# Performance work log

Measured on AMD Instinct MI355X. Metric: run time of the kernel, lower is better.

Reference implementation:

```python
import jax, jax.numpy as jnp
import numpy as np

K = 20          # knn neighbors (args.k)
BN_EPS = 1e-5   # torch BatchNorm default
LN_EPS = 1e-6


def _bn(x, g, b, axes):
    # training-mode batchnorm over `axes`, channel dim = 1
    m = x.mean(axes, keepdims=True)
    v = x.var(axes, keepdims=True)
    shp = [1] * x.ndim
    shp[1] = x.shape[1]
    return g.reshape(shp) * (x - m) * jax.lax.rsqrt(v + BN_EPS) + b.reshape(shp)


def _lrelu(x):
    return jnp.where(x >= 0, x, 0.2 * x)


def _graph_feature(x, k):
    # x: [B,C,N] -> [B,2C,N,k]  (knn gather + (neighbor-center, center) concat)
    B, C, N = x.shape
    inner = -2.0 * jnp.einsum('bcn,bcm->bnm', x, x)
    xx = jnp.sum(x * x, axis=1)                       # [B,N]
    pd = -xx[:, :, None] - inner - xx[:, None, :]     # negative sq. distance
    idx = jax.lax.top_k(pd, k)[1]                     # [B,N,k]
    xt = jnp.transpose(x, (0, 2, 1))                  # [B,N,C]
    feat = xt[jnp.arange(B)[:, None, None], idx]      # [B,N,k,C] gather
    ctr = xt[:, :, None, :]
    out = jnp.concatenate([feat - ctr, jnp.broadcast_to(ctr, feat.shape)], axis=-1)
    return jnp.transpose(out, (0, 3, 1, 2))


def _conv2d_block(x, w, g, b):
    # 1x1 conv2d (no bias) + BN2d + LeakyReLU(0.2)
    y = jnp.einsum('bcnk,oc->bonk', x, w)
    return _lrelu(_bn(y, g, b, (0, 2, 3)))


def _conv1d_block(x, w, g, b):
    y = jnp.einsum('bcl,oc->bol', x, w)
    return _lrelu(_bn(y, g, b, (0, 2)))


def _squash(t):
    sn = jnp.sum(t * t, axis=-1, keepdims=True)
    return sn * t / ((1.0 + sn) * jnp.sqrt(sn))


def _forward(data, l, dw1, dg1, db1, dw2, dg2, db2, dw3, dg3, db3,
             lin_w, ln_w, ln_b, caps_W,
             cw1, cg1, cb1, cw2, cg2, cb2, cw3, cw4, cg4, cb4, cw5, cg5, cb5):
    B, _, N = data.shape
    # ---- DGCNN encoder ----
    x = _conv2d_block(_graph_feature(data, K), dw1, dg1, db1)
    x1 = x.max(axis=-1)                               # [B,64,N]
    x = _conv2d_block(_graph_feature(x1, K), dw2, dg2, db2)
    x2 = x.max(axis=-1)                               # [B,64,N]
    x = _conv2d_block(_graph_feature(x2, K), dw3, dg3, db3)
    x3 = x.max(axis=-1)                               # [B,128,N]
    feat = jnp.transpose(jnp.concatenate([x1, x2, x3], axis=1), (0, 2, 1))  # [B,N,256]
    h = jnp.einsum('bnc,oc->bno', feat, lin_w)        # [B,N,40]
    mu = h.mean(axis=(1, 2), keepdims=True)
    var = h.var(axis=(1, 2), keepdims=True)
    encoder = jax.nn.relu(ln_w * (h - mu) * jax.lax.rsqrt(var + LN_EPS) + ln_b)  # [B,1024,40]
    # ---- Latent capsule layer (3-iter dynamic routing) ----
    u_hat = jnp.einsum('lpvd,bpd->blpv', caps_W, encoder)  # [B,40,1024,64]
    u_det = jax.lax.stop_gradient(u_hat)
    b_ij = jnp.zeros((B, caps_W.shape[0], caps_W.shape[1]), encoder.dtype)
    v = None
    for it in range(3):
        c = jax.nn.softmax(b_ij, axis=1)
        if it == 2:
            v = _squash(jnp.einsum('blp,blpv->blv', c, u_hat))
        else:
            v = _squash(jnp.einsum('blp,blpv->blv', c, u_det))
            b_ij = b_ij + jnp.einsum('blv,blpv->blp', v, u_det)
    latent = v                                        # [B,40,64]
    # ---- segmentation head ----
    emb = jnp.einsum('bpd,bdv->bpv', encoder, latent) # [B,1024,64]
    emb = emb.max(axis=-1, keepdims=True)             # [B,1024,1]
    lab = _conv1d_block(l.reshape(B, -1, 1), cw1, cg1, cb1)  # [B,64,1]
    emb = jnp.concatenate([emb, lab], axis=1)         # [B,1088,1]
    emb = jnp.tile(emb, (1, 1, N))                    # [B,1088,N]
    emb = jnp.concatenate([emb, jnp.transpose(encoder, (0, 2, 1))], axis=1)  # [B,1128,N]
    r = _conv1d_block(emb, cw2, cg2, cb2)
    r = _conv1d_block(r, cw3, cg2, cb2)               # conv3 shares bn2 params
    r = _conv1d_block(r, cw4, cg4, cb4)
    r = _conv1d_block(r, cw5, cg5, cb5)
    return r                                          # [B,50,N]


def setup_inputs() -> dict:
    key = jax.random.key(0)
    ks = jax.random.split(key, 16)
    B, N = 32, 1024
    f = jnp.float32
    rn = lambda k, s: 0.05 * jax.random.normal(k, s, dtype=f)
    return dict(
        data=jax.random.normal(ks[0], (B, 3, N), dtype=f),
        l=jax.random.uniform(ks[1], (B, 16), dtype=f),
        dw1=rn(ks[2], (64, 6)), dg1=jnp.ones(64, f), db1=jnp.zeros(64, f),
        dw2=rn(ks[3], (64, 128)), dg2=jnp.ones(64, f), db2=jnp.zeros(64, f),
        dw3=rn(ks[4], (128, 128)), dg3=jnp.ones(128, f), db3=jnp.zeros(128, f),
        lin_w=rn(ks[5], (40, 256)),
        ln_w=jnp.ones((N, 40), f), ln_b=jnp.zeros((N, 40), f),
        caps_W=0.01 * jax.random.normal(ks[6], (40, 1024, 64, 40), dtype=f),
        cw1=rn(ks[7], (64, 16)), cg1=jnp.ones(64, f), cb1=jnp.zeros(64, f),
        cw2=rn(ks[8], (256, 1128)), cg2=jnp.ones(256, f), cb2=jnp.zeros(256, f),
        cw3=rn(ks[9], (256, 256)),
        cw4=rn(ks[10], (128, 256)), cg4=jnp.ones(128, f), cb4=jnp.zeros(128, f),
        cw5=rn(ks[11], (50, 128)), cg5=jnp.ones(50, f), cb5=jnp.zeros(50, f),
    )


def reference(data, l, dw1, dg1, db1, dw2, dg2, db2, dw3, dg3, db3,
              lin_w, ln_w, ln_b, caps_W,
              cw1, cg1, cb1, cw2, cg2, cb2, cw3, cw4, cg4, cb4, cw5, cg5, cb5):
    return _forward(data, l, dw1, dg1, db1, dw2, dg2, db2, dw3, dg3, db3,
                    lin_w, ln_w, ln_b, caps_W,
                    cw1, cg1, cb1, cw2, cg2, cb2, cw3, cw4, cg4, cb4, cw5, cg5, cb5)
```

## Files before the change

### kernel.cpp

```cpp
#include <hip/hip_runtime.h>
#include <math.h>

constexpr int NB = 32, NN = 1024, KNN = 20;
constexpr int RTOT = NB * NN;

constexpr size_t SZ_BIG = (size_t)NB * NN * 40 * 64;
constexpr size_t O_BIG  = 0;
constexpr size_t O_XT0  = O_BIG + SZ_BIG;
constexpr size_t O_XT1  = O_XT0 + (size_t)RTOT * 4;
constexpr size_t O_XT2  = O_XT1 + (size_t)RTOT * 64;
constexpr size_t O_XT3  = O_XT2 + (size_t)RTOT * 64;
constexpr size_t O_XX   = O_XT3 + (size_t)RTOT * 128;
constexpr size_t O_IDX  = O_XX + RTOT;
constexpr size_t O_WC1  = O_IDX + (size_t)RTOT * KNN;
constexpr size_t O_WC2  = O_WC1 + 512;
constexpr size_t O_WC3  = O_WC2 + 8192;
constexpr size_t O_LWT  = O_WC3 + 16384;
constexpr size_t O_C2T  = O_LWT + 16384;
constexpr size_t O_C3T  = O_C2T + 10240;
constexpr size_t O_C4T  = O_C3T + 65536;
constexpr size_t O_C5T  = O_C4T + 32768;
constexpr size_t O_H    = O_C5T + 8192;
constexpr size_t O_LNST = O_H + (size_t)RTOT * 64;
constexpr size_t O_BSUM = O_LNST + 64;
constexpr size_t O_BSQ  = O_BSUM + 256;
constexpr size_t O_SCL  = O_BSQ + 256;
constexpr size_t O_SHF  = O_SCL + 256;
constexpr size_t O_SACC = O_SHF + 256;
constexpr size_t O_VB   = O_SACC + 81920;
constexpr size_t O_BIJ  = O_VB + 81920;
constexpr size_t O_EMB  = O_BIJ + (size_t)NB * 40 * NN;
constexpr size_t O_LAB  = O_EMB + RTOT;
constexpr size_t O_BASE = O_LAB + 2048;
constexpr size_t O_PS   = O_BIJ;
constexpr size_t O_PQ   = O_BIJ + 262144;
constexpr size_t O_PB   = O_XT1;
constexpr size_t O_PBU  = O_XT1;

__device__ __forceinline__ float lrelu(float z) { return fmaxf(z, 0.2f * z); }

__device__ __forceinline__ float key2f(unsigned u)
{
    unsigned b = (u & 0x80000000u) ? (u ^ 0x80000000u) : ~u;
    return __uint_as_float(b);
}

__global__ void k_wt(const float* __restrict__ src, float* __restrict__ dst,
                     int K, int On, int SS, int coff, int DS, int ooff, int Oreal)
{
    int i = blockIdx.x * 256 + threadIdx.x;
    if (i >= K * On) return;
    int c = i / On, o = i - c * On;
    dst[(size_t)c * DS + ooff + o] = (o < Oreal) ? src[(size_t)o * SS + coff + c] : 0.f;
}

__global__ void k_data_t(const float* __restrict__ d, float* __restrict__ xt)
{
    int i = blockIdx.x * 256 + threadIdx.x;
    if (i >= RTOT) return;
    int b = i >> 10, n = i & 1023;
#pragma unroll
    for (int c = 0; c < 3; ++c) xt[(size_t)i * 4 + c] = d[((size_t)b * 3 + c) * NN + n];
    xt[(size_t)i * 4 + 3] = 0.f;
}

template<int C, int CS>
__global__ void k_rownorm(const float* __restrict__ X, float* __restrict__ xx)
{
    int i = blockIdx.x * 256 + threadIdx.x;
    if (i >= RTOT) return;
    const float* p = X + (size_t)i * CS;
    float s = 0.f;
#pragma unroll
    for (int c = 0; c < C; ++c) s = fmaf(p[c], p[c], s);
    xx[i] = s;
}

template<int CS>
__global__ __launch_bounds__(256) void k_dist(const float* __restrict__ X,
    const float* __restrict__ xx, float* __restrict__ D)
{
    __shared__ float As[16][68];
    __shared__ float Bs[16][68];
    int b = blockIdx.z;
    int r0 = blockIdx.x * 64, m0 = blockIdx.y * 64;
    const float* Xb = X + (size_t)b * NN * CS;
    int t = threadIdx.x;
    int tx = t & 15, ty = t >> 4;
    float acc[4][4] = {};
    for (int k0 = 0; k0 < CS; k0 += 16) {
        __syncthreads();
        {
            int row = t >> 2, kb = (t & 3) * 4;
#pragma unroll
            for (int u = 0; u < 4; ++u) {
                int k = k0 + kb + u;
                As[kb + u][row] = (k < CS) ? Xb[(size_t)(r0 + row) * CS + k] : 0.f;
                Bs[kb + u][row] = (k < CS) ? Xb[(size_t)(m0 + row) * CS + k] : 0.f;
            }
        }
        __syncthreads();
#pragma unroll
        for (int k = 0; k < 16; ++k) {
            float4 a = *(const float4*)&As[k][ty * 4];
            float4 bb = *(const float4*)&Bs[k][tx * 4];
            float av[4] = {a.x, a.y, a.z, a.w};
            float bv[4] = {bb.x, bb.y, bb.z, bb.w};
#pragma unroll
            for (int i = 0; i < 4; ++i)
#pragma unroll
                for (int j = 0; j < 4; ++j)
                    acc[i][j] = fmaf(av[i], bv[j], acc[i][j]);
        }
    }
    const float* xxb = xx + b * NN + m0 + tx * 4;
    float x0 = xxb[0], x1 = xxb[1], x2 = xxb[2], x3 = xxb[3];
#pragma unroll
    for (int i = 0; i < 4; ++i) {
        float4 o4 = make_float4(2.f * acc[i][0] - x0, 2.f * acc[i][1] - x1,
                                2.f * acc[i][2] - x2, 2.f * acc[i][3] - x3);
        *(float4*)&D[((size_t)b * NN + r0 + ty * 4 + i) * NN + m0 + tx * 4] = o4;
    }
}

__global__ __launch_bounds__(256) void k_sel(const float* __restrict__ D,
                                             int* __restrict__ idxb)
{
    int gw = blockIdx.x * 4 + (threadIdx.x >> 6);
    int lane = threadIdx.x & 63;
    const float* drow = D + (size_t)gw * NN;
    float vr[16];
#pragma unroll
    for (int j = 0; j < 16; ++j) vr[j] = drow[j * 64 + lane];

    unsigned lo = 0x007FFFFFu;
    unsigned hi = 0xFF800000u;
#pragma unroll 1
    while (hi - lo > 1u) {
        unsigned mid = lo + ((hi - lo) >> 1);
        float tm = key2f(mid);
        int c = 0;
#pragma unroll
        for (int j = 0; j < 16; ++j) c += __popcll(__ballot(vr[j] > tm));
        if (c < KNN) hi = mid; else lo = mid;
    }
    float t = key2f(hi);

    int* outp = idxb + (size_t)gw * KNN;
    unsigned long long mylow = (1ull << lane) - 1ull;
    int base = 0;
#pragma unroll
    for (int j = 0; j < 16; ++j) {
        unsigned long long bmask = __ballot(vr[j] > t);
        if (vr[j] > t) outp[base + __popcll(bmask & mylow)] = j * 64 + lane;
        base += __popcll(bmask);
    }
#pragma unroll 1
    for (int j = 0; j < 16 && base < KNN; ++j) {
        unsigned long long bmask = __ballot(vr[j] == t);
        int pre = __popcll(bmask & mylow);
        if (vr[j] == t && base + pre < KNN) outp[base + pre] = j * 64 + lane;
        base += __popcll(bmask);
    }
}

template<bool ACT, bool BIAS>
__global__ __launch_bounds__(256) void k_gemm(const float* __restrict__ X,
    const float* __restrict__ W, float* __restrict__ Y, int K, int OC, int XS,
    const float* __restrict__ scale, const float* __restrict__ shift,
    const float* __restrict__ bias)
{
    __shared__ float Xs[16][68];
    __shared__ float Ws[16][64];
    int r0 = blockIdx.x * 64, o0 = blockIdx.y * 64;
    int t = threadIdx.x;
    int tx = t & 15, ty = t >> 4;
    float acc[4][4] = {};
    for (int k0 = 0; k0 < K; k0 += 16) {
        __syncthreads();
        {
            int row = t >> 2, kb = (t & 3) * 4;
#pragma unroll
            for (int u = 0; u < 4; ++u) {
                int k = k0 + kb + u;
                float v = 0.f;
                if (k < K) {
                    v = X[(size_t)(r0 + row) * XS + k];
                    if (ACT) { float z = fmaf(v, scale[k], shift[k]); v = fmaxf(z, 0.2f * z); }
                }
                Xs[kb + u][row] = v;
            }
            int kw = t >> 4, ow = (t & 15) * 4;
            float4 wv = make_float4(0.f, 0.f, 0.f, 0.f);
            if (k0 + kw < K) wv = *(const float4*)&W[(size_t)(k0 + kw) * OC + o0 + ow];
            *(float4*)&Ws[kw][ow] = wv;
        }
        __syncthreads();
#pragma unroll
        for (int k = 0; k < 16; ++k) {
            float4 a = *(const float4*)&Xs[k][ty * 4];
            float4 bb = *(const float4*)&Ws[k][tx * 4];
            float av[4] = {a.x, a.y, a.z, a.w};
            float bvv[4] = {bb.x, bb.y, bb.z, bb.w};
#pragma unroll
            for (int i = 0; i < 4; ++i)
#pragma unroll
                for (int j = 0; j < 4; ++j)
                    acc[i][j] = fmaf(av[i], bvv[j], acc[i][j]);
        }
    }
#pragma unroll
    for (int i = 0; i < 4; ++i) {
        int r = r0 + ty * 4 + i;
        float4 o4;
        float* po = (float*)&o4;
#pragma unroll
        for (int j = 0; j < 4; ++j) {
            float v = acc[i][j];
            if (BIAS) v += bias[(size_t)(r >> 10) * OC + o0 + tx * 4 + j];
            po[j] = v;
        }
        *(float4*)&Y[(size_t)r * OC + o0 + tx * 4] = o4;
    }
}

template<int O>
__global__ __launch_bounds__(256) void k_gather(const float* __restrict__ Z,
    const int* __restrict__ idxb, float* __restrict__ xo,
    float* __restrict__ part_s, float* __restrict__ part_q)
{
    constexpr int OL = O / 64;
    __shared__ float rs[4][O], rq[4][O];
    int b = blockIdx.y, nt = blockIdx.x;
    int t = threadIdx.x, lane = t & 63, w = t >> 6;
    float ps[OL] = {}, pq[OL] = {};
    for (int i = 0; i < 4; ++i) {
        int n = nt * 16 + w * 4 + i;
        size_t r = (size_t)b * NN + n;
        float zd[OL], ym[OL];
#pragma unroll
        for (int j = 0; j < OL; ++j) {
            int o = lane + j * 64;
            zd[j] = Z[r * (2 * O) + O + o] - Z[r * (2 * O) + o];
            ym[j] = -3.4e38f;
        }
        int midx[KNN];
        {
            const int4* ip = (const int4*)&idxb[r * KNN];
#pragma unroll
            for (int q = 0; q < 5; ++q) {
                int4 t4 = ip[q];
                midx[4 * q + 0] = t4.x; midx[4 * q + 1] = t4.y;
                midx[4 * q + 2] = t4.z; midx[4 * q + 3] = t4.w;
            }
        }
#pragma unroll
        for (int k = 0; k < KNN; ++k) {
            size_t rm = (size_t)b * NN + midx[k];
#pragma unroll
            for (int j = 0; j < OL; ++j) {
                float y = Z[rm * (2 * O) + lane + j * 64] + zd[j];
                ym[j] = fmaxf(ym[j], y);
                ps[j] += y; pq[j] = fmaf(y, y, pq[j]);
            }
        }
#pragma unroll
        for (int j = 0; j < OL; ++j) xo[r * O + lane + j * 64] = ym[j];
    }
#pragma unroll
    for (int j = 0; j < OL; ++j) { rs[w][lane + j * 64] = ps[j]; rq[w][lane + j * 64] = pq[j]; }
    __syncthreads();
    if (w == 0) {
        int blk = blockIdx.y * 64 + blockIdx.x;
#pragma unroll
        for (int j = 0; j < OL; ++j) {
            int o = lane + j * 64;
            part_s[(size_t)o * 2048 + blk] = rs[0][o] + rs[1][o] + rs[2][o] + rs[3][o];
            part_q[(size_t)o * 2048 + blk] = rq[0][o] + rq[1][o] + rq[2][o] + rq[3][o];
        }
    }
}

__global__ void k_bnfin2(const float* __restrict__ part_s, const float* __restrict__ part_q,
                         const float* __restrict__ g, const float* __restrict__ bb,
                         float* __restrict__ scale, float* __restrict__ shift,
                         int OC, float invM, float eps)
{
    int o = blockIdx.x * blockDim.x + threadIdx.x;
    if (o >= OC) return;
    const float* ps = part_s + (size_t)o * 2048;
    const float* pq = part_q + (size_t)o * 2048;
    float s0 = 0.f, s1 = 0.f, s2 = 0.f, s3 = 0.f;
    float q0 = 0.f, q1 = 0.f, q2 = 0.f, q3 = 0.f;
    for (int i = 0; i < 2048; i += 4) {
        s0 += ps[i]; s1 += ps[i + 1]; s2 += ps[i + 2]; s3 += ps[i + 3];
        q0 += pq[i]; q1 += pq[i + 1]; q2 += pq[i + 2]; q3 += pq[i + 3];
    }
    float s = (s0 + s1) + (s2 + s3);
    float q = (q0 + q1) + (q2 + q3);
    float mu = s * invM;
    float var = q * invM - mu * mu;
    float sc = g[o] * rsqrtf(var + eps);
    scale[o] = sc; shift[o] = bb[o] - mu * sc;
}

__global__ void k_bnfin(const float* __restrict__ sums, const float* __restrict__ sumsq,
                        const float* __restrict__ g, const float* __restrict__ bb,
                        float* __restrict__ scale, float* __restrict__ shift,
                        int OC, float invM, float eps)
{
    int o = blockIdx.x * blockDim.x + threadIdx.x;
    if (o >= OC) return;
    float mu = sums[o] * invM;
    float var = sumsq[o] * invM - mu * mu;
    float sc = g[o] * rsqrtf(var + eps);
    scale[o] = sc; shift[o] = bb[o] - mu * sc;
}

__global__ void k_bnapply(float* __restrict__ x, const float* __restrict__ scale,
                          const float* __restrict__ shift, int total, int O)
{
    int i = blockIdx.x * 256 + threadIdx.x;
    if (i >= total) return;
    int o = i & (O - 1);
    x[i] = lrelu(fmaf(x[i], scale[o], shift[o]));
}

__global__ void k_concat(const float* __restrict__ x1, const float* __restrict__ x2,
                         const float* __restrict__ x3, float* __restrict__ f)
{
    int i = blockIdx.x * 256 + threadIdx.x;
    if (i >= RTOT * 256) return;
    int r = i >> 8, c = i & 255;
    float v;
    if (c < 64) v = x1[(size_t)r * 64 + c];
    else if (c < 128) v = x2[(size_t)r * 64 + c - 64];
    else v = x3[(size_t)r * 128 + c - 128];
    f[(size_t)i] = v;
}

__global__ __launch_bounds__(256) void k_lnstats(const float* __restrict__ h, float* __restrict__ st)
{
    __shared__ float rsm[256], rqm[256];
    int b = blockIdx.x, t = threadIdx.x;
    float s = 0.f, q = 0.f;
    for (int i = t; i < 40960; i += 256) {
        int n = i / 40, o = i - n * 40;
        float v = h[((size_t)b * NN + n) * 64 + o];
        s += v; q = fmaf(v, v, q);
    }
    rsm[t] = s; rqm[t] = q; __syncthreads();
    for (int off = 128; off; off >>= 1) {
        if (t < off) { rsm[t] += rsm[t + off]; rqm[t] += rqm[t + off]; }
        __syncthreads();
    }
    if (t == 0) {
        float mu = rsm[0] / 40960.f;
        float var = rqm[0] / 40960.f - mu * mu;
        st[2 * b] = mu; st[2 * b + 1] = rsqrtf(var + 1e-6f);
    }
}

__global__ void k_lnapply(float* __restrict__ h, const float* __restrict__ lnw,
                          const float* __restrict__ lnb, const float* __restrict__ st)
{
    int i = blockIdx.x * 256 + threadIdx.x;
    if (i >= NB * NN * 40) return;
    int b = i / 40960, rem = i - b * 40960, n = rem / 40, o = rem - n * 40;
    float mu = st[2 * b], rstd = st[2 * b + 1];
    size_t a = ((size_t)b * NN + n) * 64 + o;
    float v = fmaf((h[a] - mu) * rstd, lnw[n * 40 + o], lnb[n * 40 + o]);
    h[a] = fmaxf(v, 0.f);
}

__global__ __launch_bounds__(128) void k_uhat(const float* __restrict__ enc,
    const float* __restrict__ caps, float* __restrict__ U, float* __restrict__ pbu)
{
    __shared__ float clt[2][40 * 68];
    __shared__ float red[2048];
    int pc = blockIdx.x, l = blockIdx.y;
    int t = threadIdx.x, lane = t & 63, wv = t >> 6;
    int vg = lane & 7, bg = lane >> 3;
    int v0 = vg * 8, b0 = bg * 4;
    float* cw = clt[wv];
    float spart[4][8] = {};
#pragma unroll 1
    for (int pi = 0; pi < 8; ++pi) {
        int p = pc * 16 + wv * 8 + pi;
        const float4* cp4 = (const float4*)(caps + ((size_t)l * NN + p) * 2560);
#pragma unroll
        for (int k = 0; k < 10; ++k) {
            int i4 = lane + k * 64;
            float4 cv = cp4[i4];
            int e0 = i4 * 4;
            int v = e0 / 40;
            int d0 = e0 - v * 40;
            cw[(d0 + 0) * 68 + v] = cv.x;
            cw[(d0 + 1) * 68 + v] = cv.y;
            cw[(d0 + 2) * 68 + v] = cv.z;
            cw[(d0 + 3) * 68 + v] = cv.w;
        }
        float acc[4][8] = {};
#pragma unroll
        for (int d4 = 0; d4 < 10; ++d4) {
            float4 e4[4];
#pragma unroll
            for (int i = 0; i < 4; ++i)
                e4[i] = *(const float4*)&enc[((size_t)(b0 + i) * NN + p) * 64 + d4 * 4];
#pragma unroll
            for (int dd = 0; dd < 4; ++dd) {
                int d = d4 * 4 + dd;
                float4 c0 = *(const float4*)&cw[d * 68 + v0];
                float4 c1 = *(const float4*)&cw[d * 68 + v0 + 4];
                float cv[8] = {c0.x, c0.y, c0.z, c0.w, c1.x, c1.y, c1.z, c1.w};
#pragma unroll
                for (int i = 0; i < 4; ++i) {
                    float e = ((const float*)&e4[i])[dd];
#pragma unroll
                    for (int j = 0; j < 8; ++j)
                        acc[i][j] = fmaf(e, cv[j], acc[i][j]);
                }
            }
        }
#pragma unroll
        for (int i = 0; i < 4; ++i) {
            float* up = &U[((size_t)(b0 + i) * NN + p) * 2560 + l * 64 + v0];
            float4 o0 = make_float4(acc[i][0], acc[i][1], acc[i][2], acc[i][3]);
            float4 o1 = make_float4(acc[i][4], acc[i][5], acc[i][6], acc[i][7]);
            *(float4*)up = o0;
            *(float4*)(up + 4) = o1;
#pragma unroll
            for (int j = 0; j < 8; ++j) spart[i][j] += acc[i][j];
        }
    }
    if (wv == 1) {
#pragma unroll
        for (int i = 0; i < 4; ++i)
#pragma unroll
            for (int j = 0; j < 8; ++j)
                red[(b0 + i) * 64 + v0 + j] = spart[i][j];
    }
    __syncthreads();
    if (wv == 0) {
        float* pb = pbu + (size_t)pc * 81920;
#pragma unroll
        for (int i = 0; i < 4; ++i)
#pragma unroll
            for (int j = 0; j < 8; ++j) {
                int bv = (b0 + i) * 64 + v0 + j;
                pb[(size_t)(b0 + i) * 2560 + l * 64 + v0 + j] = spart[i][j] + red[bv];
            }
    }
}

template<int MODE>
__global__ __launch_bounds__(256, 4) void k_route(const float* __restrict__ U,
    const float* __restrict__ vprev, const float* __restrict__ bin,
    float* __restrict__ bout, float* __restrict__ pbuf)
{
    __shared__ float vl[2560];
    __shared__ float red[4][1280];
    int b = blockIdx.x, pc = blockIdx.y;
    int t = threadIdx.x, lane = t & 63, w = t >> 6;
    for (int i = t; i < 2560; i += 256) vl[i] = vprev[(size_t)b * 2560 + i];
    __syncthreads();
    float4 acc[10];
#pragma unroll
    for (int it = 0; it < 10; ++it) acc[it] = make_float4(0.f, 0.f, 0.f, 0.f);
    int lgrp = lane >> 4;
#pragma unroll 1
    for (int pi = 0; pi < 8; ++pi) {
        int p = pc * 32 + w * 8 + pi;
        const float4* up4 = (const float4*)(U + ((size_t)b * NN + p) * 2560);
        float4 u[10];
#pragma unroll
        for (int it = 0; it < 10; ++it) u[it] = up4[it * 64 + lane];
        float pd[10];
#pragma unroll
        for (int it = 0; it < 10; ++it) {
            float4 vv = *(const float4*)&vl[it * 256 + lane * 4];
            float s = u[it].x * vv.x;
            s = fmaf(u[it].y, vv.y, s);
            s = fmaf(u[it].z, vv.z, s);
            s = fmaf(u[it].w, vv.w, s);
            s += __shfl_xor(s, 1, 64);
            s += __shfl_xor(s, 2, 64);
            s += __shfl_xor(s, 4, 64);
            s += __shfl_xor(s, 8, 64);
            pd[it] = s;
        }
        if (MODE == 1) {
            if ((lane & 15) == 0) {
#pragma unroll
                for (int it = 0; it < 10; ++it)
                    bout[((size_t)b * 40 + it * 4 + lgrp) * NN + p] = pd[it];
            }
        } else {
#pragma unroll
            for (int it = 0; it < 10; ++it)
                pd[it] += bin[((size_t)b * 40 + it * 4 + lgrp) * NN + p];
        }
        float mx = -3.4e38f;
#pragma unroll
        for (int it = 0; it < 10; ++it) {
            float m = pd[it];
            m = fmaxf(m, __shfl_xor(m, 16, 64));
            m = fmaxf(m, __shfl_xor(m, 32, 64));
            mx = fmaxf(mx, m);
        }
        float eo[10]; float se = 0.f;
#pragma unroll
        for (int it = 0; it < 10; ++it) {
            float e = expf(pd[it] - mx);
            eo[it] = e;
            float sg = e;
            sg += __shfl_xor(sg, 16, 64);
            sg += __shfl_xor(sg, 32, 64);
            se += sg;
        }
        float inv = 1.f / se;
#pragma unroll
        for (int it = 0; it < 10; ++it) {
            float wgt = eo[it] * inv;
            acc[it].x = fmaf(wgt, u[it].x, acc[it].x);
            acc[it].y = fmaf(wgt, u[it].y, acc[it].y);
            acc[it].z = fmaf(wgt, u[it].z, acc[it].z);
            acc[it].w = fmaf(wgt, u[it].w, acc[it].w);
        }
    }
    float* pb = pbuf + ((size_t)pc * NB + b) * 2560;
#pragma unroll 1
    for (int h = 0; h < 2; ++h) {
        __syncthreads();
#pragma unroll
        for (int it = 0; it < 5; ++it)
            *(float4*)&red[w][it * 256 + lane * 4] = acc[h * 5 + it];
        __syncthreads();
        if (w == 0) {
#pragma unroll
            for (int it = 0; it < 5; ++it) {
                int idx = it * 256 + lane * 4;
                float4 a0 = *(const float4*)&red[0][idx];
                float4 a1 = *(const float4*)&red[1][idx];
                float4 a2 = *(const float4*)&red[2][idx];
                float4 a3 = *(const float4*)&red[3][idx];
                float4 o = make_float4((a0.x + a1.x) + (a2.x + a3.x),
                                       (a0.y + a1.y) + (a2.y + a3.y),
                                       (a0.z + a1.z) + (a2.z + a3.z),
                                       (a0.w + a1.w) + (a2.w + a3.w));
                *(float4*)&pb[h * 1280 + idx] = o;
            }
        }
    }
}

template<int NCH>
__global__ void k_sredN(const float* __restrict__ pbuf, float* __restrict__ sac)
{
    int i4 = blockIdx.x * 256 + threadIdx.x;
    if (i4 >= NB * 640) return;
    const float4* pb4 = (const float4*)pbuf;
    float4 s = make_float4(0.f, 0.f, 0.f, 0.f);
#pragma unroll 4
    for (int pc = 0; pc < NCH; ++pc) {
        float4 v = pb4[(size_t)pc * (NB * 640) + i4];
        s.x += v.x; s.y += v.y; s.z += v.z; s.w += v.w;
    }
    ((float4*)sac)[i4] = s;
}

__global__ void k_squash(const float* __restrict__ s_in, float* __restrict__ vout, float premul)
{
    int i = blockIdx.x * 256 + threadIdx.x;
    if (i >= NB * 40) return;
    const float* sp = s_in + (size_t)i * 64;
    float* vp = vout + (size_t)i * 64;
    float sn = 0.f;
    for (int v = 0; v < 64; ++v) { float tv = sp[v] * premul; sn = fmaf(tv, tv, sn); }
    float f = sn / ((1.f + sn) * sqrtf(sn));
    for (int v = 0; v < 64; ++v) vp[v] = sp[v] * premul * f;
}

__global__ __launch_bounds__(256) void k_emb(const float* __restrict__ enc,
    const float* __restrict__ lat, float* __restrict__ embm)
{
    __shared__ float latl[2560];
    int b = blockIdx.x, pt = blockIdx.y;
    int t = threadIdx.x, lane = t & 63, w = t >> 6;
    for (int i = t; i < 2560; i += 256) latl[i] = lat[(size_t)b * 2560 + i];
    __syncthreads();
    for (int i = 0; i < 32; ++i) {
        int p = pt * 128 + w * 32 + i;
        const float* ep = enc + ((size_t)b * NN + p) * 64;
        float acc = 0.f;
#pragma unroll
        for (int d = 0; d < 40; ++d) acc = fmaf(ep[d], latl[d * 64 + lane], acc);
        float mx = acc;
#pragma unroll
        for (int s = 32; s; s >>= 1) mx = fmaxf(mx, __shfl_xor(mx, s, 64));
        if (lane == 0) embm[(size_t)b * NN + p] = mx;
    }
}

__global__ __launch_bounds__(64) void k_lab(const float* __restrict__ lin,
    const float* __restrict__ w, const float* __restrict__ g, const float* __restrict__ bb,
    float* __restrict__ lab)
{
    int o = threadIdx.x;
    float ys[32]; float s = 0.f, q = 0.f;
#pragma unroll
    for (int b = 0; b < 32; ++b) {
        float y = 0.f;
#pragma unroll
        for (int c = 0; c < 16; ++c) y = fmaf(lin[b * 16 + c], w[o * 16 + c], y);
        ys[b] = y; s += y; q = fmaf(y, y, q);
    }
    float mu = s / 32.f, var = q / 32.f - mu * mu;
    float sc = g[o] * rsqrtf(var + 1e-5f);
    float sh = bb[o] - mu * sc;
#pragma unroll
    for (int b = 0; b < 32; ++b) lab[b * 64 + o] = lrelu(fmaf(ys[b], sc, sh));
}

__global__ __launch_bounds__(256) void k_base2(const float* __restrict__ em,
    const float* __restrict__ lab, const float* __restrict__ cw2, float* __restrict__ base)
{
    __shared__ float eml[1024];
    __shared__ float lbl[64];
    int b = blockIdx.x, t = threadIdx.x;
    for (int i = t; i < 1024; i += 256) eml[i] = em[(size_t)b * NN + i];
    if (t < 64) lbl[t] = lab[b * 64 + t];
    __syncthreads();
    const float* wr = cw2 + (size_t)t * 1128;
    float acc = 0.f;
    for (int c = 0; c < 1024; ++c) acc = fmaf(wr[c], eml[c], acc);
#pragma unroll
    for (int c = 0; c < 64; ++c) acc = fmaf(wr[1024 + c], lbl[c], acc);
    base[b * 256 + t] = acc;
}

__global__ __launch_bounds__(256) void k_colstats(const float* __restrict__ Y,
    float* __restrict__ sums, float* __restrict__ sumsq, int OC)
{
    __shared__ float rs[4][64], rq[4][64];
    int chunk = blockIdx.x, o0 = blockIdx.y * 64;
    int t = threadIdx.x, lane = t & 63, w = t >> 6;
    int o = o0 + lane;
    float s = 0.f, q = 0.f;
    for (int j = 0; j < 64; ++j) {
        int r = chunk * 256 + w * 64 + j;
        float v = Y[(size_t)r * OC + o];
        s += v; q = fmaf(v, v, q);
    }
    rs[w][lane] = s; rq[w][lane] = q;
    __syncthreads();
    if (w == 0) {
        atomicAdd(&sums[o], rs[0][lane] + rs[1][lane] + rs[2][lane] + rs[3][lane]);
        atomicAdd(&sumsq[o], rq[0][lane] + rq[1][lane] + rq[2][lane] + rq[3][lane]);
    }
}

__global__ void k_out(const float* __restrict__ Y, const float* __restrict__ scale,
                      const float* __restrict__ shift, float* __restrict__ out)
{
    int i = blockIdx.x * 256 + threadIdx.x;
    if (i >= NB * 50 * NN) return;
    int n = i & 1023, rest = i >> 10;
    int o = rest % 50, b = rest / 50;
    float y = Y[((size_t)b * NN + n) * 64 + o];
    out[i] = lrelu(fmaf(y, scale[o], shift[o]));
}

extern "C" void kernel_launch(void* const* d_in, const int* in_sizes, int n_in,
                              void* d_out, int out_size, void* d_ws, size_t ws_size,
                              hipStream_t stream)
{
    const float* data = (const float*)d_in[0];
    const float* lin  = (const float*)d_in[1];
    const float* dw1  = (const float*)d_in[2];
    const float* dg1  = (const float*)d_in[3];
    const float* db1  = (const float*)d_in[4];
    const float* dw2  = (const float*)d_in[5];
    const float* dg2  = (const float*)d_in[6];
    const float* db2  = (const float*)d_in[7];
    const float* dw3  = (const float*)d_in[8];
    const float* dg3  = (const float*)d_in[9];
    const float* db3  = (const float*)d_in[10];
    const float* lw   = (const float*)d_in[11];
    const float* lnw  = (const float*)d_in[12];
    const float* lnb  = (const float*)d_in[13];
    const float* caps = (const float*)d_in[14];
    const float* cw1  = (const float*)d_in[15];
    const float* cg1  = (const float*)d_in[16];
    const float* cb1  = (const float*)d_in[17];
    const float* cw2  = (const float*)d_in[18];
    const float* cg2  = (const float*)d_in[19];
    const float* cb2  = (const float*)d_in[20];
    const float* cw3  = (const float*)d_in[21];
    const float* cw4  = (const float*)d_in[22];
    const float* cg4  = (const float*)d_in[23];
    const float* cb4  = (const float*)d_in[24];
    const float* cw5  = (const float*)d_in[25];
    const float* cg5  = (const float*)d_in[26];
    const float* cb5  = (const float*)d_in[27];
    float* out = (float*)d_out;
    float* ws = (float*)d_ws;

    float* big  = ws + O_BIG;
    float* xt0  = ws + O_XT0;
    float* xt1  = ws + O_XT1;
    float* xt2  = ws + O_XT2;
    float* xt3  = ws + O_XT3;
    float* xxp  = ws + O_XX;
    int*   idxb = (int*)(ws + O_IDX);
    float* wc1  = ws + O_WC1;
    float* wc2  = ws + O_WC2;
    float* wc3  = ws + O_WC3;
    float* lwt  = ws + O_LWT;
    float* c2t  = ws + O_C2T;
    float* c3t  = ws + O_C3T;
    float* c4t  = ws + O_C4T;
    float* c5t  = ws + O_C5T;
    float* hbuf = ws + O_H;
    float* lnst = ws + O_LNST;
    float* bsum = ws + O_BSUM;
    float* bsq  = ws + O_BSQ;
    float* scl  = ws + O_SCL;
    float* shf  = ws + O_SHF;
    float* sac  = ws + O_SACC;
    float* vb   = ws + O_VB;
    float* bij  = ws + O_BIJ;
    float* embm = ws + O_EMB;
    float* labp = ws + O_LAB;
    float* basep= ws + O_BASE;
    float* psP  = ws + O_PS;
    float* pqP  = ws + O_PQ;
    float* pbuf = ws + O_PB;
    float* pbu  = ws + O_PBU;
    float* Dbuf = big;
    float* Z    = big;
    float* U    = big;
    float* yb1  = big;
    float* yb2  = big + 8388608;

    k_wt<<<1,   256, 0, stream>>>(dw1, wc1, 3, 64, 6, 0, 128, 0, 64);
    k_wt<<<1,   256, 0, stream>>>(dw1, wc1, 3, 64, 6, 3, 128, 64, 64);
    k_wt<<<16,  256, 0, stream>>>(dw2, wc2, 64, 64, 128, 0, 128, 0, 64);
    k_wt<<<16,  256, 0, stream>>>(dw2, wc2, 64, 64, 128, 64, 128, 64, 64);
    k_wt<<<32,  256, 0, stream>>>(dw3, wc3, 64, 128, 128, 0, 256, 0, 128);
    k_wt<<<32,  256, 0, stream>>>(dw3, wc3, 64, 128, 128, 64, 256, 128, 128);
    k_wt<<<64,  256, 0, stream>>>(lw,  lwt, 256, 64, 256, 0, 64, 0, 40);
    k_wt<<<40,  256, 0, stream>>>(cw2, c2t, 40, 256, 1128, 1088, 256, 0, 256);
    k_wt<<<256, 256, 0, stream>>>(cw3, c3t, 256, 256, 256, 0, 256, 0, 256);
    k_wt<<<128, 256, 0, stream>>>(cw4, c4t, 256, 128, 256, 0, 128, 0, 128);
    k_wt<<<32,  256, 0, stream>>>(cw5, c5t, 128, 64, 128, 0, 64, 0, 50);
    k_data_t<<<128, 256, 0, stream>>>(data, xt0);

    k_rownorm<3, 4><<<128, 256, 0, stream>>>(xt0, xxp);
    k_dist<4><<<dim3(16, 16, 32), 256, 0, stream>>>(xt0, xxp, Dbuf);
    k_sel<<<8192, 256, 0, stream>>>(Dbuf, idxb);
    k_gemm<false, false><<<dim3(512, 2), 256, 0, stream>>>(xt0, wc1, Z, 3, 128, 4, nullptr, nullptr, nullptr);
    k_gather<64><<<dim3(64, 32), 256, 0, stream>>>(Z, idxb, xt1, psP, pqP);
    k_bnfin2<<<1, 64, 0, stream>>>(psP, pqP, dg1, db1, scl, shf, 64, 1.f / 655360.f, 1e-5f);
    k_bnapply<<<8192, 256, 0, stream>>>(xt1, scl, shf, RTOT * 64, 64);

    k_rownorm<64, 64><<<128, 256, 0, stream>>>(xt1, xxp);
    k_dist<64><<<dim3(16, 16, 32), 256, 0, stream>>>(xt1, xxp, Dbuf);
    k_sel<<<8192, 256, 0, stream>>>(Dbuf, idxb);
    k_gemm<false, false><<<dim3(512, 2), 256, 0, stream>>>(xt1, wc2, Z, 64, 128, 64, nullptr, nullptr, nullptr);
    k_gather<64><<<dim3(64, 32), 256, 0, stream>>>(Z, idxb, xt2, psP, pqP);
    k_bnfin2<<<1, 64, 0, stream>>>(psP, pqP, dg2, db2, scl, shf, 64, 1.f / 655360.f, 1e-5f);
    k_bnapply<<<8192, 256, 0, stream>>>(xt2, scl, shf, RTOT * 64, 64);

    k_rownorm<64, 64><<<128, 256, 0, stream>>>(xt2, xxp);
    k_dist<64><<<dim3(16, 16, 32), 256, 0, stream>>>(xt2, xxp, Dbuf);
    k_sel<<<8192, 256, 0, stream>>>(Dbuf, idxb);
    k_gemm<false, false><<<dim3(512, 4), 256, 0, stream>>>(xt2, wc3, Z, 64, 256, 64, nullptr, nullptr, nullptr);
    k_gather<128><<<dim3(64, 32), 256, 0, stream>>>(Z, idxb, xt3, psP, pqP);
    k_bnfin2<<<1, 128, 0, stream>>>(psP, pqP, dg3, db3, scl, shf, 128, 1.f / 655360.f, 1e-5f);
    k_bnapply<<<16384, 256, 0, stream>>>(xt3, scl, shf, RTOT * 128, 128);

    k_concat<<<32768, 256, 0, stream>>>(xt1, xt2, xt3, big);
    k_gemm<false, false><<<dim3(512, 1), 256, 0, stream>>>(big, lwt, hbuf, 256, 64, 256, nullptr, nullptr, nullptr);
    k_lnstats<<<32, 256, 0, stream>>>(hbuf, lnst);
    k_lnapply<<<5120, 256, 0, stream>>>(hbuf, lnw, lnb, lnst);

    k_uhat<<<dim3(64, 40), 128, 0, stream>>>(hbuf, caps, U, pbu);
    k_sredN<64><<<80, 256, 0, stream>>>(pbu, sac);
    k_squash<<<5, 256, 0, stream>>>(sac, vb, 1.f / 40.f);
    k_route<1><<<dim3(32, 32), 256, 0, stream>>>(U, vb, nullptr, bij, pbuf);
    k_sredN<32><<<80, 256, 0, stream>>>(pbuf, sac);
    k_squash<<<5, 256, 0, stream>>>(sac, vb, 1.f);
    k_route<2><<<dim3(32, 32), 256, 0, stream>>>(U, vb, bij, nullptr, pbuf);
    k_sredN<32><<<80, 256, 0, stream>>>(pbuf, sac);
    k_squash<<<5, 256, 0, stream>>>(sac, vb, 1.f);

    k_emb<<<dim3(32, 8), 256, 0, stream>>>(hbuf, vb, embm);
    k_lab<<<1, 64, 0, stream>>>(lin, cw1, cg1, cb1, labp);
    k_base2<<<32, 256, 0, stream>>>(embm, labp, cw2, basep);

    k_gemm<false, true><<<dim3(512, 4), 256, 0, stream>>>(hbuf, c2t, yb1, 40, 256, 64, nullptr, nullptr, basep);
    hipMemsetAsync(bsum, 0, 512 * 4, stream);
    k_colstats<<<dim3(128, 4), 256, 0, stream>>>(yb1, bsum, bsq, 256);
    k_bnfin<<<1, 256, 0, stream>>>(bsum, bsq, cg2, cb2, scl, shf, 256, 1.f / 32768.f, 1e-5f);

    k_gemm<true, false><<<dim3(512, 4), 256, 0, stream>>>(yb1, c3t, yb2, 256, 256, 256, scl, shf, nullptr);
    hipMemsetAsync(bsum, 0, 512 * 4, stream);
    k_colstats<<<dim3(128, 4), 256, 0, stream>>>(yb2, bsum, bsq, 256);
    k_bnfin<<<1, 256, 0, stream>>>(bsum, bsq, cg2, cb2, scl, shf, 256, 1.f / 32768.f, 1e-5f);

    k_gemm<true, false><<<dim3(512, 2), 256, 0, stream>>>(yb2, c4t, yb1, 256, 128, 256, scl, shf, nullptr);
    hipMemsetAsync(bsum, 0, 512 * 4, stream);
    k_colstats<<<dim3(128, 2), 256, 0, stream>>>(yb1, bsum, bsq, 128);
    k_bnfin<<<1, 256, 0, stream>>>(bsum, bsq, cg4, cb4, scl, shf, 128, 1.f / 32768.f, 1e-5f);

    k_gemm<true, false><<<dim3(512, 1), 256, 0, stream>>>(yb1, c5t, yb2, 128, 64, 128, scl, shf, nullptr);
    hipMemsetAsync(bsum, 0, 512 * 4, stream);
    k_colstats<<<dim3(128, 1), 256, 0, stream>>>(yb2, bsum, bsq, 64);
    k_bnfin<<<1, 256, 0, stream>>>(bsum, bsq, cg5, cb5, scl, shf, 50, 1.f / 32768.f, 1e-5f);

    k_out<<<6400, 256, 0, stream>>>(yb2, scl, shf, out);
}
```

Before: 1.765 ms.

## Fuse kNN distance computation with top-k selection in shared memory

Replaces the separate tiled distance GEMM and the top-k selection kernel with one kernel. Each block computes distance rows for 8 points into shared memory and then runs the existing ballot-based threshold search on them. This removes writing and re-reading a full B×N×N distance matrix in global memory for each of the three graph layers. In exchange, the distance computation loses the 2D register tiling, so every block streams all candidate points from cache, which raises L2 traffic and lowers arithmetic reuse.

```diff
diff --git a/kernel.cpp b/kernel.cpp
--- a/kernel.cpp
+++ b/kernel.cpp
@@ -76,91 +76,74 @@
     xx[i] = s;
 }
 
-template<int CS>
-__global__ __launch_bounds__(256) void k_dist(const float* __restrict__ X,
-    const float* __restrict__ xx, float* __restrict__ D)
-{
-    __shared__ float As[16][68];
-    __shared__ float Bs[16][68];
-    int b = blockIdx.z;
-    int r0 = blockIdx.x * 64, m0 = blockIdx.y * 64;
+template<int CS, int CV>
+__global__ __launch_bounds__(256) void k_dsel(const float* __restrict__ X,
+    const float* __restrict__ xx, int* __restrict__ idxb)
+{
+    __shared__ float dist[8][1024];
+    __shared__ float rows8[8][CV];
+    int b = blockIdx.y, n0 = blockIdx.x * 8;
+    int t = threadIdx.x, lane = t & 63, w = t >> 6;
     const float* Xb = X + (size_t)b * NN * CS;
-    int t = threadIdx.x;
-    int tx = t & 15, ty = t >> 4;
-    float acc[4][4] = {};
-    for (int k0 = 0; k0 < CS; k0 += 16) {
-        __syncthreads();
-        {
-            int row = t >> 2, kb = (t & 3) * 4;
-#pragma unroll
-            for (int u = 0; u < 4; ++u) {
-                int k = k0 + kb + u;
-                As[kb + u][row] = (k < CS) ? Xb[(size_t)(r0 + row) * CS + k] : 0.f;
-                Bs[kb + u][row] = (k < CS) ? Xb[(size_t)(m0 + row) * CS + k] : 0.f;
-            }
-        }
-        __syncthreads();
-#pragma unroll
-        for (int k = 0; k < 16; ++k) {
-            float4 a = *(const float4*)&As[k][ty * 4];
-            float4 bb = *(const float4*)&Bs[k][tx * 4];
-            float av[4] = {a.x, a.y, a.z, a.w};
-            float bv[4] = {bb.x, bb.y, bb.z, bb.w};
-#pragma unroll
-            for (int i = 0; i < 4; ++i)
-#pragma unroll
-                for (int j = 0; j < 4; ++j)
-                    acc[i][j] = fmaf(av[i], bv[j], acc[i][j]);
-        }
-    }
-    const float* xxb = xx + b * NN + m0 + tx * 4;
-    float x0 = xxb[0], x1 = xxb[1], x2 = xxb[2], x3 = xxb[3];
-#pragma unroll
-    for (int i = 0; i < 4; ++i) {
-        float4 o4 = make_float4(2.f * acc[i][0] - x0, 2.f * acc[i][1] - x1,
-                                2.f * acc[i][2] - x2, 2.f * acc[i][3] - x3);
-        *(float4*)&D[((size_t)b * NN + r0 + ty * 4 + i) * NN + m0 + tx * 4] = o4;
-    }
-}
-
-__global__ __launch_bounds__(256) void k_sel(const float* __restrict__ D,
-                                             int* __restrict__ idxb)
-{
-    int gw = blockIdx.x * 4 + (threadIdx.x >> 6);
-    int lane = threadIdx.x & 63;
-    const float* drow = D + (size_t)gw * NN;
-    float vr[16];
-#pragma unroll
-    for (int j = 0; j < 16; ++j) vr[j] = drow[j * 64 + lane];
-
-    unsigned lo = 0x007FFFFFu;
-    unsigned hi = 0xFF800000u;
+    for (int i = t; i < 8 * CV; i += 256)
+        rows8[i / CV][i % CV] = Xb[(size_t)(n0 + i / CV) * CS + (i % CV)];
+    __syncthreads();
+    const float* xxb = xx + b * NN;
 #pragma unroll 1
-    while (hi - lo > 1u) {
-        unsigned mid = lo + ((hi - lo) >> 1);
-        float tm = key2f(mid);
-        int c = 0;
-#pragma unroll
-        for (int j = 0; j < 16; ++j) c += __popcll(__ballot(vr[j] > tm));
-        if (c < KNN) hi = mid; else lo = mid;
-    }
-    float t = key2f(hi);
-
-    int* outp = idxb + (size_t)gw * KNN;
-    unsigned long long mylow = (1ull << lane) - 1ull;
-    int base = 0;
-#pragma unroll
-    for (int j = 0; j < 16; ++j) {
-        unsigned long long bmask = __ballot(vr[j] > t);
-        if (vr[j] > t) outp[base + __popcll(bmask & mylow)] = j * 64 + lane;
-        base += __popcll(bmask);
+    for (int mt = 0; mt < 16; ++mt) {
+        int m = mt * 64 + lane;
+        const float* xmp = Xb + (size_t)m * CS;
+        float acc0 = 0.f, acc1 = 0.f;
+#pragma unroll
+        for (int c4 = 0; c4 < CV / 4; ++c4) {
+            float4 xm = *(const float4*)(xmp + 4 * c4);
+            float4 aa = *(const float4*)(&rows8[2 * w][4 * c4]);
+            float4 bb = *(const float4*)(&rows8[2 * w + 1][4 * c4]);
+            acc0 = fmaf(aa.x, xm.x, acc0); acc0 = fmaf(aa.y, xm.y, acc0);
+            acc0 = fmaf(aa.z, xm.z, acc0); acc0 = fmaf(aa.w, xm.w, acc0);
+            acc1 = fmaf(bb.x, xm.x, acc1); acc1 = fmaf(bb.y, xm.y, acc1);
+            acc1 = fmaf(bb.z, xm.z, acc1); acc1 = fmaf(bb.w, xm.w, acc1);
+        }
+        float xxm = xxb[m];
+        dist[2 * w][m] = 2.f * acc0 - xxm;
+        dist[2 * w + 1][m] = 2.f * acc1 - xxm;
     }
 #pragma unroll 1
-    for (int j = 0; j < 16 && base < KNN; ++j) {
-        unsigned long long bmask = __ballot(vr[j] == t);
-        int pre = __popcll(bmask & mylow);
-        if (vr[j] == t && base + pre < KNN) outp[base + pre] = j * 64 + lane;
-        base += __popcll(bmask);
+    for (int rr = 0; rr < 2; ++rr) {
+        int row = 2 * w + rr;
+        float vr[16];
+#pragma unroll
+        for (int j = 0; j < 16; ++j) vr[j] = dist[row][j * 64 + lane];
+
+        unsigned lo = 0x007FFFFFu;
+        unsigned hi = 0xFF800000u;
+#pragma unroll 1
+        while (hi - lo > 1u) {
+            unsigned mid = lo + ((hi - lo) >> 1);
+            float tm = key2f(mid);
+            int c = 0;
+#pragma unroll
+            for (int j = 0; j < 16; ++j) c += __popcll(__ballot(vr[j] > tm));
+            if (c < KNN) hi = mid; else lo = mid;
+        }
+        float tv = key2f(hi);
+
+        int* outp = idxb + ((size_t)b * NN + n0 + row) * KNN;
+        unsigned long long mylow = (1ull << lane) - 1ull;
+        int base = 0;
+#pragma unroll
+        for (int j = 0; j < 16; ++j) {
+            unsigned long long bmask = __ballot(vr[j] > tv);
+            if (vr[j] > tv) outp[base + __popcll(bmask & mylow)] = j * 64 + lane;
+            base += __popcll(bmask);
+        }
+#pragma unroll 1
+        for (int j = 0; j < 16 && base < KNN; ++j) {
+            unsigned long long bmask = __ballot(vr[j] == tv);
+            int pre = __popcll(bmask & mylow);
+            if (vr[j] == tv && base + pre < KNN) outp[base + pre] = j * 64 + lane;
+            base += __popcll(bmask);
+        }
     }
 }
 
@@ -737,7 +720,6 @@
     float* pqP  = ws + O_PQ;
     float* pbuf = ws + O_PB;
     float* pbu  = ws + O_PBU;
-    float* Dbuf = big;
     float* Z    = big;
     float* U    = big;
     float* yb1  = big;
@@ -757,24 +739,21 @@
     k_data_t<<<128, 256, 0, stream>>>(data, xt0);
 
     k_rownorm<3, 4><<<128, 256, 0, stream>>>(xt0, xxp);
-    k_dist<4><<<dim3(16, 16, 32), 256, 0, stream>>>(xt0, xxp, Dbuf);
-    k_sel<<<8192, 256, 0, stream>>>(Dbuf, idxb);
+    k_dsel<4, 4><<<dim3(128, 32), 256, 0, stream>>>(xt0, xxp, idxb);
     k_gemm<false, false><<<dim3(512, 2), 256, 0, stream>>>(xt0, wc1, Z, 3, 128, 4, nullptr, nullptr, nullptr);
     k_gather<64><<<dim3(64, 32), 256, 0, stream>>>(Z, idxb, xt1, psP, pqP);
     k_bnfin2<<<1, 64, 0, stream>>>(psP, pqP, dg1, db1, scl, shf, 64, 1.f / 655360.f, 1e-5f);
     k_bnapply<<<8192, 256, 0, stream>>>(xt1, scl, shf, RTOT * 64, 64);
 
     k_rownorm<64, 64><<<128, 256, 0, stream>>>(xt1, xxp);
-    k_dist<64><<<dim3(16, 16, 32), 256, 0, stream>>>(xt1, xxp, Dbuf);
-    k_sel<<<8192, 256, 0, stream>>>(Dbuf, idxb);
+    k_dsel<64, 64><<<dim3(128, 32), 256, 0, stream>>>(xt1, xxp, idxb);
     k_gemm<false, false><<<dim3(512, 2), 256, 0, stream>>>(xt1, wc2, Z, 64, 128, 64, nullptr, nullptr, nullptr);
     k_gather<64><<<dim3(64, 32), 256, 0, stream>>>(Z, idxb, xt2, psP, pqP);
     k_bnfin2<<<1, 64, 0, stream>>>(psP, pqP, dg2, db2, scl, shf, 64, 1.f / 655360.f, 1e-5f);
     k_bnapply<<<8192, 256, 0, stream>>>(xt2, scl, shf, RTOT * 64, 64);
 
     k_rownorm<64, 64><<<128, 256, 0, stream>>>(xt2, xxp);
-    k_dist<64><<<dim3(16, 16, 32), 256, 0, stream>>>(xt2, xxp, Dbuf);
-    k_sel<<<8192, 256, 0, stream>>>(Dbuf, idxb);
+    k_dsel<64, 64><<<dim3(128, 32), 256, 0, stream>>>(xt2, xxp, idxb);
     k_gemm<false, false><<<dim3(512, 4), 256, 0, stream>>>(xt2, wc3, Z, 64, 256, 64, nullptr, nullptr, nullptr);
     k_gather<128><<<dim3(64, 32), 256, 0, stream>>>(Z, idxb, xt3, psP, pqP);
     k_bnfin2<<<1, 128, 0, stream>>>(psP, pqP, dg3, db3, scl, shf, 128, 1.f / 655360.f, 1e-5f);
```

Result: slower. 3.073 ms (+74.1%).
